# Optimization experiments

Measured on AMD Instinct MI355X. Metric: run time of the kernel, lower is better.

Reference implementation:

```python
import jax, jax.numpy as jnp
import numpy as np

N = 131072       # total nodes (B graphs x P nodes)
P = 4096         # nodes per graph
B = 32           # graphs in batch
E = 2097152      # edges (avg degree 16)
IN_DIM = 64
HID = 128
OUT = 16
EPS = 1e-5
SLOPE = 0.01


def _degrees(idx):
    # structural degree, clamped to min 1 (as DGL GraphConv does)
    d = jax.ops.segment_sum(jnp.ones((E,), jnp.float32), idx, num_segments=N)
    return jnp.maximum(d, 1.0)


def _graph_conv(x, W, src, dst, ew):
    # DGL GraphConv, norm='both', bias=False, with scalar edge weights:
    # h = D_out^{-1/2} x ; m_v = sum_{(u->v)} w_e h_u ; out = (D_in^{-1/2} m) W
    h = x * jax.lax.rsqrt(_degrees(src))[:, None]
    m = jax.ops.segment_sum(ew[:, None] * h[src], dst, num_segments=N)  # [N, F]
    return (m * jax.lax.rsqrt(_degrees(dst))[:, None]) @ W


def _graph_norm(x, gamma, beta, alpha):
    # GraphNorm (Cai et al. / PyG, batch=None): stats over all nodes per feature
    mu = jnp.mean(x, axis=0)
    c = x - alpha * mu
    var = jnp.mean(c * c, axis=0)
    return c * jax.lax.rsqrt(var + EPS) * gamma + beta


def _mean_nodes(h, gid):
    # per-graph mean readout; every graph has exactly P nodes
    return jax.ops.segment_sum(h, gid, num_segments=B) / P


def setup_inputs() -> dict:
    key = jax.random.key(0)
    ks = jax.random.split(key, 8)
    src = jax.random.randint(ks[0], (E,), 0, N, dtype=jnp.int32)
    # keep edges within each 4096-node graph block (batched DGL graph)
    dst = (src // P) * P + jax.random.randint(ks[1], (E,), 0, P, dtype=jnp.int32)
    features = jax.random.normal(ks[2], (N, IN_DIM), jnp.float32)
    edge_weights = jax.random.uniform(ks[3], (E,), jnp.float32)
    # kaiming/xavier-scale init approximations
    W1 = jax.random.normal(ks[4], (IN_DIM, HID), jnp.float32) * np.sqrt(2.0 / IN_DIM)
    W2 = jax.random.normal(ks[5], (HID, HID), jnp.float32) * np.sqrt(2.0 / HID)
    Wc = jax.random.normal(ks[6], (OUT, 2 * HID), jnp.float32) * np.sqrt(1.0 / (2 * HID))
    ones = jnp.ones((HID,), jnp.float32)
    zeros = jnp.zeros((HID,), jnp.float32)
    return {
        'features': features, 'edge_weights': edge_weights, 'src': src, 'dst': dst,
        'W1': W1, 'W2': W2, 'Wc': Wc,
        'gamma1': ones, 'beta1': zeros, 'alpha1': ones,
        'gamma2': ones, 'beta2': zeros, 'alpha2': ones,
    }


def reference(features, edge_weights, src, dst, W1, W2, Wc,
              gamma1, beta1, alpha1, gamma2, beta2, alpha2):
    gid = jnp.arange(N, dtype=jnp.int32) // P  # node -> graph id
    h1 = _graph_conv(features, W1, src, dst, edge_weights)
    h1 = jax.nn.leaky_relu(_graph_norm(h1, gamma1, beta1, alpha1), SLOPE)
    r1 = _mean_nodes(h1, gid)                  # [B, HID]
    h2 = _graph_conv(h1, W2, src, dst, edge_weights)
    h2 = jax.nn.leaky_relu(_graph_norm(h2, gamma2, beta2, alpha2), SLOPE)
    r2 = _mean_nodes(h2, gid)                  # [B, HID]
    readouts = jnp.concatenate([r1, r2], axis=1)  # [B, 2*HID]
    return readouts @ Wc.T                     # [B, OUT]
```

## Files before the change

### kernel.cpp

```cpp
#include <hip/hip_runtime.h>
#include <hip/hip_fp16.h>

constexpr int NN   = 131072;
constexpr int PP   = 4096;
constexpr int BG   = 32;
constexpr int EE   = 2097152;
constexpr int IND  = 64;
constexpr int HH   = 128;
constexpr int CAP  = 81920;
constexpr float EPSV   = 1e-5f;
constexpr float SLOPEV = 0.01f;

typedef short bf16x8 __attribute__((ext_vector_type(8)));
typedef float f32x4  __attribute__((ext_vector_type(4)));

__device__ __forceinline__ unsigned f2bf(float f) {
    unsigned u = __float_as_uint(f);
    return (u + 0x7FFFu + ((u >> 16) & 1u)) >> 16;
}
__device__ __forceinline__ unsigned pack2bf(float lo, float hi) {
    return f2bf(lo) | (f2bf(hi) << 16);
}
__device__ __forceinline__ float bflo(unsigned p) { return __uint_as_float(p << 16); }
__device__ __forceinline__ float bfhi(unsigned p) { return __uint_as_float(p & 0xFFFF0000u); }
__device__ __forceinline__ float w16(unsigned r) {
    return __half2float(__ushort_as_half((unsigned short)(r >> 16)));
}

template <int K>
__device__ __forceinline__ void packw_body(const float* __restrict__ W,
                                           unsigned short* __restrict__ pw, int t) {
    if (t >= K * 16) return;
    int lane = t & 63, nt = (t >> 6) & 7, kt = t >> 9;
    int kbase = kt * 32 + ((lane >> 4) & 3) * 8;
    int col   = nt * 16 + (lane & 15);
    for (int j = 0; j < 8; j++)
        pw[t * 8 + j] = (unsigned short)f2bf(W[(kbase + j) * HH + col]);
}

__global__ __launch_bounds__(256) void k_prep(const float* __restrict__ features,
                                              unsigned* __restrict__ fx,
                                              const float* __restrict__ W1,
                                              unsigned short* __restrict__ pw1,
                                              const float* __restrict__ W2,
                                              unsigned short* __restrict__ pw2,
                                              int* __restrict__ gcur,
                                              float* __restrict__ racc) {
    int b = blockIdx.x, t = threadIdx.x;
    if (b < 16384) {
        int i = b * 256 + t;
        float2 v = ((const float2*)features)[i];
        fx[i] = pack2bf(v.x, v.y);
        return;
    }
    if (b == 16384) {
        if (t < BG) gcur[t * 16] = t * CAP;
        for (int i = t; i < 2 * BG * HH; i += 256) racc[i] = 0.f;
        return;
    }
    if (b < 16389) { packw_body<64>(W1, pw1, (b - 16385) * 256 + t); return; }
    packw_body<128>(W2, pw2, (b - 16389) * 256 + t);
}

__global__ __launch_bounds__(256) void k_part(const int* __restrict__ src,
                                              const int* __restrict__ dst,
                                              const float* __restrict__ ew,
                                              int* __restrict__ gcur,
                                              uint2* __restrict__ recs) {
    __shared__ int cnt[32];
    __shared__ int start[32];
    __shared__ int gbase[32];
    __shared__ uint2 stage[4096];
    int t = threadIdx.x;
    int ebase = blockIdx.x * 4096;
    if (t < 32) cnt[t] = 0;
    __syncthreads();
    int es[16]; int ed[16]; float ev[16];
#pragma unroll
    for (int k = 0; k < 16; k++) {
        int e = ebase + k * 256 + t;
        es[k] = src[e]; ed[k] = dst[e]; ev[k] = ew[e];
        atomicAdd(&cnt[es[k] >> 12], 1);
    }
    __syncthreads();
    if (t == 0) {
        int run = 0;
        for (int g = 0; g < 32; g++) { start[g] = run; run += cnt[g]; }
    }
    __syncthreads();
    if (t < 32) {
        gbase[t] = atomicAdd(&gcur[t * 16], cnt[t]);
        cnt[t] = start[t];
    }
    __syncthreads();
#pragma unroll
    for (int k = 0; k < 16; k++) {
        int g = es[k] >> 12;
        int pos = atomicAdd(&cnt[g], 1);
        stage[pos] = make_uint2((unsigned)(es[k] & 4095) | ((unsigned)(ed[k] & 4095) << 12) |
                                ((unsigned)g << 24), __float_as_uint(ev[k]));
    }
    __syncthreads();
    for (int i = t; i < 4096; i += 256) {
        uint2 r = stage[i];
        int g = r.x >> 24;
        recs[gbase[g] + (i - start[g])] = r;
    }
}

__global__ __launch_bounds__(1024) void k_hist(const uint2* __restrict__ recs,
                                               const int* __restrict__ gcur,
                                               int* __restrict__ shist,
                                               int* __restrict__ dhist) {
    __shared__ int hs[4096];
    __shared__ int hd[4096];
    int t = threadIdx.x;
    int g = blockIdx.x >> 3, c = blockIdx.x & 7;
    int n = gcur[g * 16] - g * CAP;
    int lo = (n * c) >> 3, hi = (n * (c + 1)) >> 3;
    ((int4*)hs)[t] = make_int4(0, 0, 0, 0);
    ((int4*)hd)[t] = make_int4(0, 0, 0, 0);
    __syncthreads();
    const uint2* base = recs + (size_t)g * CAP;
    for (int i = lo + t; i < hi; i += 1024) {
        unsigned x = base[i].x;
        atomicAdd(&hs[x & 4095], 1);
        atomicAdd(&hd[(x >> 12) & 4095], 1);
    }
    __syncthreads();
    ((int4*)(shist + (size_t)blockIdx.x * 4096))[t] = ((int4*)hs)[t];
    ((int4*)(dhist + (size_t)blockIdx.x * 4096))[t] = ((int4*)hd)[t];
}

__global__ __launch_bounds__(1024) void k_offs(int* __restrict__ shist,
                                               int* __restrict__ dhist,
                                               float* __restrict__ rs_s,
                                               float* __restrict__ rsd,
                                               int* __restrict__ degd,
                                               int* __restrict__ offs) {
    __shared__ int partial[1024];
    int t = threadIdx.x, g = blockIdx.x;
    int sdeg[4] = {0, 0, 0, 0}, ddeg[4] = {0, 0, 0, 0};
#pragma unroll
    for (int c = 0; c < 8; c++) {
        int4 sv = ((const int4*)(shist + (size_t)(g * 8 + c) * 4096))[t];
        int4 dv = ((const int4*)(dhist + (size_t)(g * 8 + c) * 4096))[t];
        sdeg[0] += sv.x; sdeg[1] += sv.y; sdeg[2] += sv.z; sdeg[3] += sv.w;
        ddeg[0] += dv.x; ddeg[1] += dv.y; ddeg[2] += dv.z; ddeg[3] += dv.w;
    }
    int pdeg[4];
#pragma unroll
    for (int j = 0; j < 4; j++) {
        int idx = t * 4 + j;
        int vs = sdeg[j]; if (vs < 1) vs = 1;
        rs_s[g * PP + idx] = rsqrtf((float)vs);
        int vd = ddeg[j]; if (vd < 1) vd = 1;
        rsd[g * PP + idx]  = rsqrtf((float)vd);
        pdeg[j] = (ddeg[j] + 3) & ~3;
        degd[g * PP + idx] = pdeg[j];
    }
    partial[t] = pdeg[0] + pdeg[1] + pdeg[2] + pdeg[3];
    __syncthreads();
    for (int off = 1; off < 1024; off <<= 1) {
        int v = partial[t];
        int add = (t >= off) ? partial[t - off] : 0;
        __syncthreads();
        partial[t] = v + add;
        __syncthreads();
    }
    int run = (t == 0) ? 0 : partial[t - 1];
#pragma unroll
    for (int j = 0; j < 4; j++) {
        int idx = t * 4 + j;
        offs[g * PP + idx] = g * CAP + run;
        int nb = run;
        for (int c = 0; c < 8; c++) {
            size_t hidx = (size_t)(g * 8 + c) * 4096 + idx;
            int v = dhist[hidx];
            dhist[hidx] = nb;
            nb += v;
        }
        run += pdeg[j];
    }
}

__global__ __launch_bounds__(1024) void k_place(const uint2* __restrict__ recs,
                                                const int* __restrict__ gcur,
                                                const int* __restrict__ dhist,
                                                const float* __restrict__ rs_s,
                                                unsigned* __restrict__ csr2) {
    __shared__ int cur[4096];
    __shared__ float rss[4096];
    int t = threadIdx.x;
    int g = blockIdx.x >> 3, c = blockIdx.x & 7;
    int n = gcur[g * 16] - g * CAP;
    int lo = (n * c) >> 3, hi = (n * (c + 1)) >> 3;
    ((int4*)cur)[t] = ((const int4*)(dhist + (size_t)blockIdx.x * 4096))[t];
    ((float4*)rss)[t] = ((const float4*)(rs_s + (size_t)g * PP))[t];
    __syncthreads();
    const uint2* base = recs + (size_t)g * CAP;
    unsigned* cbase = csr2 + (size_t)g * CAP;
    for (int i = lo + t; i < hi; i += 1024) {
        uint2 r = base[i];
        int sl = r.x & 4095, dl = (r.x >> 12) & 4095;
        int pos = atomicAdd(&cur[dl], 1);
        float wf = __uint_as_float(r.y) * rss[sl];
        cbase[pos] = (unsigned)sl | ((unsigned)__half_as_ushort(__float2half(wf)) << 16);
    }
}

__global__ __launch_bounds__(256) void k_agg1(const unsigned* __restrict__ fx,
                                              const unsigned* __restrict__ csr2,
                                              const int* __restrict__ offs,
                                              const int* __restrict__ degd,
                                              const float* __restrict__ rsd,
                                              unsigned* __restrict__ m1) {
    int bid = blockIdx.x;
    int xcd = bid & 7, idx = bid >> 3;
    int g = xcd * 4 + (idx >> 9);
    int node0 = g * PP + (idx & 511) * 8;
    int lane = threadIdx.x & 63, wv = threadIdx.x >> 6;
    int half = lane >> 5, sl = lane & 31;
    int v = node0 + wv * 2 + half;
    int o = offs[v], cnt = degd[v];
    const unsigned* hp = fx + (size_t)((unsigned)(g * PP) * 32) + sl;
    float ax0 = 0.f, ay0 = 0.f, ax1 = 0.f, ay1 = 0.f;
    for (int i = 0; i < cnt; i += 4) {
        uint4 rr = *(const uint4*)(csr2 + o + i);
        unsigned g0 = hp[(rr.x & 4095) * 32];
        unsigned g1 = hp[(rr.y & 4095) * 32];
        unsigned g2 = hp[(rr.z & 4095) * 32];
        unsigned g3 = hp[(rr.w & 4095) * 32];
        float w0 = w16(rr.x), w1 = w16(rr.y), w2 = w16(rr.z), w3 = w16(rr.w);
        ax0 += w0 * bflo(g0); ay0 += w0 * bfhi(g0);
        ax1 += w1 * bflo(g1); ay1 += w1 * bfhi(g1);
        ax0 += w2 * bflo(g2); ay0 += w2 * bfhi(g2);
        ax1 += w3 * bflo(g3); ay1 += w3 * bfhi(g3);
    }
    float rd = rsd[v];
    m1[(size_t)v * 32 + sl] = pack2bf((ax0 + ax1) * rd, (ay0 + ay1) * rd);
}

__global__ __launch_bounds__(256) void k_agg2(const unsigned* __restrict__ h1,
                                              const unsigned* __restrict__ csr2,
                                              const int* __restrict__ offs,
                                              const int* __restrict__ degd,
                                              const float* __restrict__ rsd,
                                              unsigned* __restrict__ m2) {
    int bid = blockIdx.x;
    int xcd = bid & 7, idx = bid >> 3;
    int g = xcd * 4 + (idx >> 9);
    int node0 = g * PP + (idx & 511) * 4;
    int lane = threadIdx.x & 63, wv = threadIdx.x >> 6;
    int va = node0 + wv, vb = va + 2048;
    int oa = offs[va], ca = degd[va];
    int ob = offs[vb], cb = degd[vb];
    const unsigned* hp = h1 + (size_t)((unsigned)(g * PP) * 64) + lane;
    float A0 = 0.f, A1 = 0.f, B0 = 0.f, B1 = 0.f;
    int c0 = ca < cb ? ca : cb;
    int cm = ca < cb ? cb : ca;
    int i = 0;
    for (; i < c0; i += 4) {
        uint4 ra = *(const uint4*)(csr2 + oa + i);
        uint4 rb = *(const uint4*)(csr2 + ob + i);
        unsigned ga0 = hp[(ra.x & 4095) * 64];
        unsigned ga1 = hp[(ra.y & 4095) * 64];
        unsigned ga2 = hp[(ra.z & 4095) * 64];
        unsigned ga3 = hp[(ra.w & 4095) * 64];
        unsigned gb0 = hp[(rb.x & 4095) * 64];
        unsigned gb1 = hp[(rb.y & 4095) * 64];
        unsigned gb2 = hp[(rb.z & 4095) * 64];
        unsigned gb3 = hp[(rb.w & 4095) * 64];
        float wa0 = w16(ra.x), wa1 = w16(ra.y), wa2 = w16(ra.z), wa3 = w16(ra.w);
        float wb0 = w16(rb.x), wb1 = w16(rb.y), wb2 = w16(rb.z), wb3 = w16(rb.w);
        A0 += wa0 * bflo(ga0); A1 += wa0 * bfhi(ga0);
        A0 += wa1 * bflo(ga1); A1 += wa1 * bfhi(ga1);
        A0 += wa2 * bflo(ga2); A1 += wa2 * bfhi(ga2);
        A0 += wa3 * bflo(ga3); A1 += wa3 * bfhi(ga3);
        B0 += wb0 * bflo(gb0); B1 += wb0 * bfhi(gb0);
        B0 += wb1 * bflo(gb1); B1 += wb1 * bfhi(gb1);
        B0 += wb2 * bflo(gb2); B1 += wb2 * bfhi(gb2);
        B0 += wb3 * bflo(gb3); B1 += wb3 * bfhi(gb3);
    }
    if (i < cm) {
        int ot = (ca > cb) ? oa : ob;
        float E0 = 0.f, E1 = 0.f, F0 = 0.f, F1 = 0.f;
        for (; i < cm; i += 4) {
            uint4 rr = *(const uint4*)(csr2 + ot + i);
            unsigned g0 = hp[(rr.x & 4095) * 64];
            unsigned g1 = hp[(rr.y & 4095) * 64];
            unsigned g2 = hp[(rr.z & 4095) * 64];
            unsigned g3 = hp[(rr.w & 4095) * 64];
            float w0 = w16(rr.x), w1 = w16(rr.y), w2 = w16(rr.z), w3 = w16(rr.w);
            E0 += w0 * bflo(g0); E1 += w0 * bfhi(g0);
            F0 += w1 * bflo(g1); F1 += w1 * bfhi(g1);
            E0 += w2 * bflo(g2); E1 += w2 * bfhi(g2);
            F0 += w3 * bflo(g3); F1 += w3 * bfhi(g3);
        }
        if (ca > cb) { A0 += E0 + F0; A1 += E1 + F1; }
        else         { B0 += E0 + F0; B1 += E1 + F1; }
    }
    float rda = rsd[va], rdb = rsd[vb];
    m2[(size_t)va * 64 + lane] = pack2bf(A0 * rda, A1 * rda);
    m2[(size_t)vb * 64 + lane] = pack2bf(B0 * rdb, B1 * rdb);
}

template <int K>
__global__ __launch_bounds__(256) void k_gemm(const short* __restrict__ A,
                                              const short* __restrict__ PW,
                                              unsigned short* __restrict__ C,
                                              float* __restrict__ part) {
    __shared__ float s1[HH], s2[HH];
    int t = threadIdx.x;
    if (t < HH) { s1[t] = 0.f; s2[t] = 0.f; }
    __syncthreads();
    int wv = t >> 6, lane = t & 63;
    int tile = blockIdx.x * 4 + wv;
    int m = lane & 15, quad = lane >> 4;
    int row = tile * 16 + m;
    bf16x8 a[K / 32];
#pragma unroll
    for (int kt = 0; kt < K / 32; kt++)
        a[kt] = *(const bf16x8*)(A + (size_t)row * K + kt * 32 + quad * 8);
#pragma unroll
    for (int nt = 0; nt < 8; nt++) {
        f32x4 acc = {0.f, 0.f, 0.f, 0.f};
#pragma unroll
        for (int kt = 0; kt < K / 32; kt++) {
            bf16x8 b = *(const bf16x8*)(PW + ((size_t)(kt * 8 + nt) * 64 + lane) * 8);
            acc = __builtin_amdgcn_mfma_f32_16x16x32_bf16(a[kt], b, acc, 0, 0, 0);
        }
        int col = nt * 16 + m;
        int r0 = tile * 16 + quad * 4;
        float ps = 0.f, pq = 0.f;
#pragma unroll
        for (int r = 0; r < 4; r++) {
            C[(size_t)(r0 + r) * HH + col] = (unsigned short)f2bf(acc[r]);
            ps += acc[r]; pq += acc[r] * acc[r];
        }
        atomicAdd(&s1[col], ps);
        atomicAdd(&s2[col], pq);
    }
    __syncthreads();
    if (t < HH) {
        part[blockIdx.x * 256 + t]      = s1[t];
        part[blockIdx.x * 256 + HH + t] = s2[t];
    }
}

__global__ __launch_bounds__(256) void k_red(const float* __restrict__ part,
                                             float* __restrict__ pb) {
    int t = threadIdx.x, b = blockIdx.x;
    float s = 0.f;
    for (int r = 0; r < 32; r++) s += part[(size_t)(b * 32 + r) * 256 + t];
    pb[b * 256 + t] = s;
}

__global__ void k_coef(const float* __restrict__ pb, const float* __restrict__ gamma,
                       const float* __restrict__ beta, const float* __restrict__ alpha,
                       float* __restrict__ ab) {
    int t = threadIdx.x;
    float s = 0.f;
    for (int b = 0; b < 64; b++) s += pb[b * 256 + t];
    __shared__ float sh[256];
    sh[t] = s;
    __syncthreads();
    if (t < 128) {
        float mu = sh[t] * (1.f / NN);
        float e2 = sh[128 + t] * (1.f / NN);
        float al = alpha[t];
        float var = e2 - (2.f * al - al * al) * mu * mu;
        float a = rsqrtf(var + EPSV) * gamma[t];
        ab[t] = a;
        ab[HH + t] = beta[t] - al * mu * a;
    }
}

template <bool WRITE>
__global__ __launch_bounds__(256) void k_normro(unsigned* __restrict__ h,
                                                const float* __restrict__ ab,
                                                float* __restrict__ racc) {
    int fp = threadIdx.x & 63;
    int q  = threadIdx.x >> 6;
    int node0 = blockIdx.x * 64;
    int g = node0 / PP;
    float a0 = ab[2 * fp], a1 = ab[2 * fp + 1];
    float b0 = ab[HH + 2 * fp], b1 = ab[HH + 2 * fp + 1];
    float s0 = 0.f, s1 = 0.f;
    for (int i = q; i < 64; i += 4) {
        size_t idx = (size_t)(node0 + i) * 64 + fp;
        unsigned v = h[idx];
        float x0 = fmaf(a0, bflo(v), b0); x0 = x0 > 0.f ? x0 : SLOPEV * x0;
        float x1 = fmaf(a1, bfhi(v), b1); x1 = x1 > 0.f ? x1 : SLOPEV * x1;
        if (WRITE) h[idx] = pack2bf(x0, x1);
        s0 += x0; s1 += x1;
    }
    __shared__ float sh[512];
    sh[threadIdx.x] = s0;
    sh[256 + threadIdx.x] = s1;
    __syncthreads();
    if (q == 0) {
        float t0 = s0 + sh[64 + fp] + sh[128 + fp] + sh[192 + fp];
        float t1 = s1 + sh[256 + 64 + fp] + sh[256 + 128 + fp] + sh[256 + 192 + fp];
        atomicAdd(&racc[g * HH + 2 * fp],     t0);
        atomicAdd(&racc[g * HH + 2 * fp + 1], t1);
    }
}

__global__ void k_final(const float* __restrict__ racc1, const float* __restrict__ racc2,
                        const float* __restrict__ Wc, float* __restrict__ out) {
    int t = threadIdx.x;
    int b = t >> 4, o = t & 15;
    float acc = 0.f;
    for (int f = 0; f < HH; f++) acc += racc1[b * HH + f] * Wc[o * (2 * HH) + f];
    for (int f = 0; f < HH; f++) acc += racc2[b * HH + f] * Wc[o * (2 * HH) + HH + f];
    out[t] = acc * (1.f / PP);
}

extern "C" void kernel_launch(void* const* d_in, const int* in_sizes, int n_in,
                              void* d_out, int out_size, void* d_ws, size_t ws_size,
                              hipStream_t stream) {
    const float* features = (const float*)d_in[0];
    const float* ew       = (const float*)d_in[1];
    const int*   src      = (const int*)d_in[2];
    const int*   dst      = (const int*)d_in[3];
    const float* W1       = (const float*)d_in[4];
    const float* W2       = (const float*)d_in[5];
    const float* Wc       = (const float*)d_in[6];
    const float* gamma1   = (const float*)d_in[7];
    const float* beta1    = (const float*)d_in[8];
    const float* alpha1   = (const float*)d_in[9];
    const float* gamma2   = (const float*)d_in[10];
    const float* beta2    = (const float*)d_in[11];
    const float* alpha2   = (const float*)d_in[12];
    float* out = (float*)d_out;

    char* w = (char*)d_ws;
    int*    gcur   = (int*)(w + 0);
    float*  racc1  = (float*)(w + (16u << 10));
    float*  racc2  = (float*)(w + (32u << 10));
    float*  ab1    = (float*)(w + (48u << 10));
    float*  ab2    = (float*)(w + (52u << 10));
    unsigned short* pw1 = (unsigned short*)(w + (64u << 10));
    unsigned short* pw2 = (unsigned short*)(w + (80u << 10));
    float*  pb     = (float*)(w + (128u << 10));
    float*  rs_s   = (float*)(w + (1024u << 10));
    float*  rsd    = (float*)(w + (1536u << 10));
    int*    degd   = (int*)(w + (2048u << 10));
    int*    offs   = (int*)(w + (2560u << 10));
    float*  part   = (float*)(w + (3u << 20));
    int*    shist  = (int*)(w + (5u << 20));
    int*    dhist  = (int*)(w + (9u << 20));
    unsigned* csr2 = (unsigned*)(w + (13u << 20));
    unsigned* mbuf = (unsigned*)(w + (23u << 20));
    unsigned* hbuf = (unsigned*)(w + (55u << 20));
    uint2*    recs = (uint2*)(w + (87u << 20));
    unsigned* fx   = (unsigned*)(w + (107u << 20));

    k_prep<<<16397, 256, 0, stream>>>(features, fx, W1, pw1, W2, pw2, gcur, racc1);
    hipMemsetAsync(csr2, 0, (size_t)BG * CAP * sizeof(unsigned), stream);

    k_part<<<EE / 4096, 256, 0, stream>>>(src, dst, ew, gcur, recs);
    k_hist<<<BG * 8, 1024, 0, stream>>>(recs, gcur, shist, dhist);
    k_offs<<<BG, 1024, 0, stream>>>(shist, dhist, rs_s, rsd, degd, offs);
    k_place<<<BG * 8, 1024, 0, stream>>>(recs, gcur, dhist, rs_s, csr2);

    k_agg1<<<NN / 8, 256, 0, stream>>>(fx, csr2, offs, degd, rsd, mbuf);
    k_gemm<64><<<NN / 64, 256, 0, stream>>>((const short*)mbuf, (const short*)pw1,
                                            (unsigned short*)hbuf, part);
    k_red<<<64, 256, 0, stream>>>(part, pb);
    k_coef<<<1, 256, 0, stream>>>(pb, gamma1, beta1, alpha1, ab1);
    k_normro<true><<<NN / 64, 256, 0, stream>>>(hbuf, ab1, racc1);

    k_agg2<<<NN / 8, 256, 0, stream>>>(hbuf, csr2, offs, degd, rsd, mbuf);
    k_gemm<128><<<NN / 64, 256, 0, stream>>>((const short*)mbuf, (const short*)pw2,
                                             (unsigned short*)hbuf, part);
    k_red<<<64, 256, 0, stream>>>(part, pb);
    k_coef<<<1, 256, 0, stream>>>(pb, gamma2, beta2, alpha2, ab2);
    k_normro<false><<<NN / 64, 256, 0, stream>>>(hbuf, ab2, racc2);

    k_final<<<1, 512, 0, stream>>>(racc1, racc2, Wc, out);
}
```

Baseline: 412.8 us.

## Fuse neighbor aggregation with MFMA GEMM via LDS staging, fold csr2 memset into prep

Aggregation and the dense weight GEMM now run in one kernel per layer. Each block aggregates 64 nodes into a padded LDS tile and then runs bf16 MFMA directly from LDS, so the intermediate aggregated buffer no longer goes through global memory. The second layer writes to mbuf so that hbuf, which it reads from, is not overwritten. The csr2 zeroing moves from hipMemsetAsync into extra blocks of the prep kernel. In exchange the grid is 8x smaller, and each wave walks 8 sequential node groups, which lowers the parallelism available to hide gather latency.

```diff
diff --git a/kernel.cpp b/kernel.cpp
--- a/kernel.cpp
+++ b/kernel.cpp
@@ -45,7 +45,8 @@
                                               const float* __restrict__ W2,
                                               unsigned short* __restrict__ pw2,
                                               int* __restrict__ gcur,
-                                              float* __restrict__ racc) {
+                                              float* __restrict__ racc,
+                                              unsigned* __restrict__ csr2) {
     int b = blockIdx.x, t = threadIdx.x;
     if (b < 16384) {
         int i = b * 256 + t;
@@ -59,7 +60,8 @@
         return;
     }
     if (b < 16389) { packw_body<64>(W1, pw1, (b - 16385) * 256 + t); return; }
-    packw_body<128>(W2, pw2, (b - 16389) * 256 + t);
+    if (b < 16397) { packw_body<128>(W2, pw2, (b - 16389) * 256 + t); return; }
+    ((uint4*)csr2)[(b - 16397) * 256 + t] = make_uint4(0, 0, 0, 0);
 }
 
 __global__ __launch_bounds__(256) void k_part(const int* __restrict__ src,
@@ -209,129 +211,62 @@
     }
 }
 
-__global__ __launch_bounds__(256) void k_agg1(const unsigned* __restrict__ fx,
-                                              const unsigned* __restrict__ csr2,
-                                              const int* __restrict__ offs,
-                                              const int* __restrict__ degd,
-                                              const float* __restrict__ rsd,
-                                              unsigned* __restrict__ m1) {
+__global__ __launch_bounds__(256) void k_aggemm1(const unsigned* __restrict__ fx,
+                                                 const unsigned* __restrict__ csr2,
+                                                 const int* __restrict__ offs,
+                                                 const int* __restrict__ degd,
+                                                 const float* __restrict__ rsd,
+                                                 const short* __restrict__ PW,
+                                                 unsigned short* __restrict__ C,
+                                                 float* __restrict__ part) {
+    constexpr int WP = 36;
+    __shared__ unsigned lds[64 * WP];
+    __shared__ float s1[HH], s2[HH];
+    int t = threadIdx.x;
+    if (t < HH) { s1[t] = 0.f; s2[t] = 0.f; }
     int bid = blockIdx.x;
     int xcd = bid & 7, idx = bid >> 3;
-    int g = xcd * 4 + (idx >> 9);
-    int node0 = g * PP + (idx & 511) * 8;
-    int lane = threadIdx.x & 63, wv = threadIdx.x >> 6;
+    int g = xcd * 4 + (idx >> 6);
+    int node0 = g * PP + (idx & 63) * 64;
+    int lane = t & 63, wv = t >> 6;
     int half = lane >> 5, sl = lane & 31;
-    int v = node0 + wv * 2 + half;
-    int o = offs[v], cnt = degd[v];
     const unsigned* hp = fx + (size_t)((unsigned)(g * PP) * 32) + sl;
-    float ax0 = 0.f, ay0 = 0.f, ax1 = 0.f, ay1 = 0.f;
-    for (int i = 0; i < cnt; i += 4) {
-        uint4 rr = *(const uint4*)(csr2 + o + i);
-        unsigned g0 = hp[(rr.x & 4095) * 32];
-        unsigned g1 = hp[(rr.y & 4095) * 32];
-        unsigned g2 = hp[(rr.z & 4095) * 32];
-        unsigned g3 = hp[(rr.w & 4095) * 32];
-        float w0 = w16(rr.x), w1 = w16(rr.y), w2 = w16(rr.z), w3 = w16(rr.w);
-        ax0 += w0 * bflo(g0); ay0 += w0 * bfhi(g0);
-        ax1 += w1 * bflo(g1); ay1 += w1 * bfhi(g1);
-        ax0 += w2 * bflo(g2); ay0 += w2 * bfhi(g2);
-        ax1 += w3 * bflo(g3); ay1 += w3 * bfhi(g3);
-    }
-    float rd = rsd[v];
-    m1[(size_t)v * 32 + sl] = pack2bf((ax0 + ax1) * rd, (ay0 + ay1) * rd);
-}
-
-__global__ __launch_bounds__(256) void k_agg2(const unsigned* __restrict__ h1,
-                                              const unsigned* __restrict__ csr2,
-                                              const int* __restrict__ offs,
-                                              const int* __restrict__ degd,
-                                              const float* __restrict__ rsd,
-                                              unsigned* __restrict__ m2) {
-    int bid = blockIdx.x;
-    int xcd = bid & 7, idx = bid >> 3;
-    int g = xcd * 4 + (idx >> 9);
-    int node0 = g * PP + (idx & 511) * 4;
-    int lane = threadIdx.x & 63, wv = threadIdx.x >> 6;
-    int va = node0 + wv, vb = va + 2048;
-    int oa = offs[va], ca = degd[va];
-    int ob = offs[vb], cb = degd[vb];
-    const unsigned* hp = h1 + (size_t)((unsigned)(g * PP) * 64) + lane;
-    float A0 = 0.f, A1 = 0.f, B0 = 0.f, B1 = 0.f;
-    int c0 = ca < cb ? ca : cb;
-    int cm = ca < cb ? cb : ca;
-    int i = 0;
-    for (; i < c0; i += 4) {
-        uint4 ra = *(const uint4*)(csr2 + oa + i);
-        uint4 rb = *(const uint4*)(csr2 + ob + i);
-        unsigned ga0 = hp[(ra.x & 4095) * 64];
-        unsigned ga1 = hp[(ra.y & 4095) * 64];
-        unsigned ga2 = hp[(ra.z & 4095) * 64];
-        unsigned ga3 = hp[(ra.w & 4095) * 64];
-        unsigned gb0 = hp[(rb.x & 4095) * 64];
-        unsigned gb1 = hp[(rb.y & 4095) * 64];
-        unsigned gb2 = hp[(rb.z & 4095) * 64];
-        unsigned gb3 = hp[(rb.w & 4095) * 64];
-        float wa0 = w16(ra.x), wa1 = w16(ra.y), wa2 = w16(ra.z), wa3 = w16(ra.w);
-        float wb0 = w16(rb.x), wb1 = w16(rb.y), wb2 = w16(rb.z), wb3 = w16(rb.w);
-        A0 += wa0 * bflo(ga0); A1 += wa0 * bfhi(ga0);
-        A0 += wa1 * bflo(ga1); A1 += wa1 * bfhi(ga1);
-        A0 += wa2 * bflo(ga2); A1 += wa2 * bfhi(ga2);
-        A0 += wa3 * bflo(ga3); A1 += wa3 * bfhi(ga3);
-        B0 += wb0 * bflo(gb0); B1 += wb0 * bfhi(gb0);
-        B0 += wb1 * bflo(gb1); B1 += wb1 * bfhi(gb1);
-        B0 += wb2 * bflo(gb2); B1 += wb2 * bfhi(gb2);
-        B0 += wb3 * bflo(gb3); B1 += wb3 * bfhi(gb3);
-    }
-    if (i < cm) {
-        int ot = (ca > cb) ? oa : ob;
-        float E0 = 0.f, E1 = 0.f, F0 = 0.f, F1 = 0.f;
-        for (; i < cm; i += 4) {
-            uint4 rr = *(const uint4*)(csr2 + ot + i);
-            unsigned g0 = hp[(rr.x & 4095) * 64];
-            unsigned g1 = hp[(rr.y & 4095) * 64];
-            unsigned g2 = hp[(rr.z & 4095) * 64];
-            unsigned g3 = hp[(rr.w & 4095) * 64];
+    for (int p = 0; p < 8; p++) {
+        int lr = wv * 16 + p * 2 + half;
+        int v = node0 + lr;
+        int o = offs[v], cnt = degd[v];
+        float ax0 = 0.f, ay0 = 0.f, ax1 = 0.f, ay1 = 0.f;
+        for (int i = 0; i < cnt; i += 4) {
+            uint4 rr = *(const uint4*)(csr2 + o + i);
+            unsigned g0 = hp[(rr.x & 4095) * 32];
+            unsigned g1 = hp[(rr.y & 4095) * 32];
+            unsigned g2 = hp[(rr.z & 4095) * 32];
+            unsigned g3 = hp[(rr.w & 4095) * 32];
             float w0 = w16(rr.x), w1 = w16(rr.y), w2 = w16(rr.z), w3 = w16(rr.w);
-            E0 += w0 * bflo(g0); E1 += w0 * bfhi(g0);
-            F0 += w1 * bflo(g1); F1 += w1 * bfhi(g1);
-            E0 += w2 * bflo(g2); E1 += w2 * bfhi(g2);
-            F0 += w3 * bflo(g3); F1 += w3 * bfhi(g3);
-        }
-        if (ca > cb) { A0 += E0 + F0; A1 += E1 + F1; }
-        else         { B0 += E0 + F0; B1 += E1 + F1; }
-    }
-    float rda = rsd[va], rdb = rsd[vb];
-    m2[(size_t)va * 64 + lane] = pack2bf(A0 * rda, A1 * rda);
-    m2[(size_t)vb * 64 + lane] = pack2bf(B0 * rdb, B1 * rdb);
-}
-
-template <int K>
-__global__ __launch_bounds__(256) void k_gemm(const short* __restrict__ A,
-                                              const short* __restrict__ PW,
-                                              unsigned short* __restrict__ C,
-                                              float* __restrict__ part) {
-    __shared__ float s1[HH], s2[HH];
-    int t = threadIdx.x;
-    if (t < HH) { s1[t] = 0.f; s2[t] = 0.f; }
-    __syncthreads();
-    int wv = t >> 6, lane = t & 63;
-    int tile = blockIdx.x * 4 + wv;
+            ax0 += w0 * bflo(g0); ay0 += w0 * bfhi(g0);
+            ax1 += w1 * bflo(g1); ay1 += w1 * bfhi(g1);
+            ax0 += w2 * bflo(g2); ay0 += w2 * bfhi(g2);
+            ax1 += w3 * bflo(g3); ay1 += w3 * bfhi(g3);
+        }
+        float rd = rsd[v];
+        lds[lr * WP + sl] = pack2bf((ax0 + ax1) * rd, (ay0 + ay1) * rd);
+    }
+    __syncthreads();
     int m = lane & 15, quad = lane >> 4;
-    int row = tile * 16 + m;
-    bf16x8 a[K / 32];
-#pragma unroll
-    for (int kt = 0; kt < K / 32; kt++)
-        a[kt] = *(const bf16x8*)(A + (size_t)row * K + kt * 32 + quad * 8);
+    bf16x8 a[2];
+#pragma unroll
+    for (int kt = 0; kt < 2; kt++)
+        a[kt] = *(const bf16x8*)&lds[(wv * 16 + m) * WP + kt * 16 + quad * 4];
 #pragma unroll
     for (int nt = 0; nt < 8; nt++) {
         f32x4 acc = {0.f, 0.f, 0.f, 0.f};
 #pragma unroll
-        for (int kt = 0; kt < K / 32; kt++) {
+        for (int kt = 0; kt < 2; kt++) {
             bf16x8 b = *(const bf16x8*)(PW + ((size_t)(kt * 8 + nt) * 64 + lane) * 8);
             acc = __builtin_amdgcn_mfma_f32_16x16x32_bf16(a[kt], b, acc, 0, 0, 0);
         }
         int col = nt * 16 + m;
-        int r0 = tile * 16 + quad * 4;
+        int r0 = node0 + wv * 16 + quad * 4;
         float ps = 0.f, pq = 0.f;
 #pragma unroll
         for (int r = 0; r < 4; r++) {
@@ -343,8 +278,111 @@
     }
     __syncthreads();
     if (t < HH) {
-        part[blockIdx.x * 256 + t]      = s1[t];
-        part[blockIdx.x * 256 + HH + t] = s2[t];
+        part[bid * 256 + t]      = s1[t];
+        part[bid * 256 + HH + t] = s2[t];
+    }
+}
+
+__global__ __launch_bounds__(256) void k_aggemm2(const unsigned* __restrict__ h1,
+                                                 const unsigned* __restrict__ csr2,
+                                                 const int* __restrict__ offs,
+                                                 const int* __restrict__ degd,
+                                                 const float* __restrict__ rsd,
+                                                 const short* __restrict__ PW,
+                                                 unsigned short* __restrict__ C,
+                                                 float* __restrict__ part) {
+    constexpr int WP = 68;
+    __shared__ unsigned lds[64 * WP];
+    __shared__ float s1[HH], s2[HH];
+    int t = threadIdx.x;
+    if (t < HH) { s1[t] = 0.f; s2[t] = 0.f; }
+    int bid = blockIdx.x;
+    int xcd = bid & 7, idx = bid >> 3;
+    int g = xcd * 4 + (idx >> 6);
+    int node0 = g * PP + (idx & 63) * 64;
+    int lane = t & 63, wv = t >> 6;
+    const unsigned* hp = h1 + (size_t)((unsigned)(g * PP) * 64) + lane;
+    for (int p = 0; p < 8; p++) {
+        int va = node0 + wv * 16 + p, vb = va + 8;
+        int oa = offs[va], ca = degd[va];
+        int ob = offs[vb], cb = degd[vb];
+        float A0 = 0.f, A1 = 0.f, B0 = 0.f, B1 = 0.f;
+        int c0 = ca < cb ? ca : cb;
+        int cm = ca < cb ? cb : ca;
+        int i = 0;
+        for (; i < c0; i += 4) {
+            uint4 ra = *(const uint4*)(csr2 + oa + i);
+            uint4 rb = *(const uint4*)(csr2 + ob + i);
+            unsigned ga0 = hp[(ra.x & 4095) * 64];
+            unsigned ga1 = hp[(ra.y & 4095) * 64];
+            unsigned ga2 = hp[(ra.z & 4095) * 64];
+            unsigned ga3 = hp[(ra.w & 4095) * 64];
+            unsigned gb0 = hp[(rb.x & 4095) * 64];
+            unsigned gb1 = hp[(rb.y & 4095) * 64];
+            unsigned gb2 = hp[(rb.z & 4095) * 64];
+            unsigned gb3 = hp[(rb.w & 4095) * 64];
+            float wa0 = w16(ra.x), wa1 = w16(ra.y), wa2 = w16(ra.z), wa3 = w16(ra.w);
+            float wb0 = w16(rb.x), wb1 = w16(rb.y), wb2 = w16(rb.z), wb3 = w16(rb.w);
+            A0 += wa0 * bflo(ga0); A1 += wa0 * bfhi(ga0);
+            A0 += wa1 * bflo(ga1); A1 += wa1 * bfhi(ga1);
+            A0 += wa2 * bflo(ga2); A1 += wa2 * bfhi(ga2);
+            A0 += wa3 * bflo(ga3); A1 += wa3 * bfhi(ga3);
+            B0 += wb0 * bflo(gb0); B1 += wb0 * bfhi(gb0);
+            B0 += wb1 * bflo(gb1); B1 += wb1 * bfhi(gb1);
+            B0 += wb2 * bflo(gb2); B1 += wb2 * bfhi(gb2);
+            B0 += wb3 * bflo(gb3); B1 += wb3 * bfhi(gb3);
+        }
+        if (i < cm) {
+            int ot = (ca > cb) ? oa : ob;
+            float E0 = 0.f, E1 = 0.f, F0 = 0.f, F1 = 0.f;
+            for (; i < cm; i += 4) {
+                uint4 rr = *(const uint4*)(csr2 + ot + i);
+                unsigned g0 = hp[(rr.x & 4095) * 64];
+                unsigned g1 = hp[(rr.y & 4095) * 64];
+                unsigned g2 = hp[(rr.z & 4095) * 64];
+                unsigned g3 = hp[(rr.w & 4095) * 64];
+                float w0 = w16(rr.x), w1 = w16(rr.y), w2 = w16(rr.z), w3 = w16(rr.w);
+                E0 += w0 * bflo(g0); E1 += w0 * bfhi(g0);
+                F0 += w1 * bflo(g1); F1 += w1 * bfhi(g1);
+                E0 += w2 * bflo(g2); E1 += w2 * bfhi(g2);
+                F0 += w3 * bflo(g3); F1 += w3 * bfhi(g3);
+            }
+            if (ca > cb) { A0 += E0 + F0; A1 += E1 + F1; }
+            else         { B0 += E0 + F0; B1 += E1 + F1; }
+        }
+        float rda = rsd[va], rdb = rsd[vb];
+        lds[(wv * 16 + p) * WP + lane]     = pack2bf(A0 * rda, A1 * rda);
+        lds[(wv * 16 + p + 8) * WP + lane] = pack2bf(B0 * rdb, B1 * rdb);
+    }
+    __syncthreads();
+    int m = lane & 15, quad = lane >> 4;
+    bf16x8 a[4];
+#pragma unroll
+    for (int kt = 0; kt < 4; kt++)
+        a[kt] = *(const bf16x8*)&lds[(wv * 16 + m) * WP + kt * 16 + quad * 4];
+#pragma unroll
+    for (int nt = 0; nt < 8; nt++) {
+        f32x4 acc = {0.f, 0.f, 0.f, 0.f};
+#pragma unroll
+        for (int kt = 0; kt < 4; kt++) {
+            bf16x8 b = *(const bf16x8*)(PW + ((size_t)(kt * 8 + nt) * 64 + lane) * 8);
+            acc = __builtin_amdgcn_mfma_f32_16x16x32_bf16(a[kt], b, acc, 0, 0, 0);
+        }
+        int col = nt * 16 + m;
+        int r0 = node0 + wv * 16 + quad * 4;
+        float ps = 0.f, pq = 0.f;
+#pragma unroll
+        for (int r = 0; r < 4; r++) {
+            C[(size_t)(r0 + r) * HH + col] = (unsigned short)f2bf(acc[r]);
+            ps += acc[r]; pq += acc[r] * acc[r];
+        }
+        atomicAdd(&s1[col], ps);
+        atomicAdd(&s2[col], pq);
+    }
+    __syncthreads();
+    if (t < HH) {
+        part[bid * 256 + t]      = s1[t];
+        part[bid * 256 + HH + t] = s2[t];
     }
 }
 
@@ -457,27 +495,24 @@
     uint2*    recs = (uint2*)(w + (87u << 20));
     unsigned* fx   = (unsigned*)(w + (107u << 20));
 
-    k_prep<<<16397, 256, 0, stream>>>(features, fx, W1, pw1, W2, pw2, gcur, racc1);
-    hipMemsetAsync(csr2, 0, (size_t)BG * CAP * sizeof(unsigned), stream);
+    k_prep<<<18957, 256, 0, stream>>>(features, fx, W1, pw1, W2, pw2, gcur, racc1, csr2);
 
     k_part<<<EE / 4096, 256, 0, stream>>>(src, dst, ew, gcur, recs);
     k_hist<<<BG * 8, 1024, 0, stream>>>(recs, gcur, shist, dhist);
     k_offs<<<BG, 1024, 0, stream>>>(shist, dhist, rs_s, rsd, degd, offs);
     k_place<<<BG * 8, 1024, 0, stream>>>(recs, gcur, dhist, rs_s, csr2);
 
-    k_agg1<<<NN / 8, 256, 0, stream>>>(fx, csr2, offs, degd, rsd, mbuf);
-    k_gemm<64><<<NN / 64, 256, 0, stream>>>((const short*)mbuf, (const short*)pw1,
-                                            (unsigned short*)hbuf, part);
+    k_aggemm1<<<NN / 64, 256, 0, stream>>>(fx, csr2, offs, degd, rsd,
+                                           (const short*)pw1, (unsigned short*)hbuf, part);
     k_red<<<64, 256, 0, stream>>>(part, pb);
     k_coef<<<1, 256, 0, stream>>>(pb, gamma1, beta1, alpha1, ab1);
     k_normro<true><<<NN / 64, 256, 0, stream>>>(hbuf, ab1, racc1);
 
-    k_agg2<<<NN / 8, 256, 0, stream>>>(hbuf, csr2, offs, degd, rsd, mbuf);
-    k_gemm<128><<<NN / 64, 256, 0, stream>>>((const short*)mbuf, (const short*)pw2,
-                                             (unsigned short*)hbuf, part);
+    k_aggemm2<<<NN / 64, 256, 0, stream>>>(hbuf, csr2, offs, degd, rsd,
+                                           (const short*)pw2, (unsigned short*)mbuf, part);
     k_red<<<64, 256, 0, stream>>>(part, pb);
     k_coef<<<1, 256, 0, stream>>>(pb, gamma2, beta2, alpha2, ab2);
-    k_normro<false><<<NN / 64, 256, 0, stream>>>(hbuf, ab2, racc2);
+    k_normro<false><<<NN / 64, 256, 0, stream>>>(mbuf, ab2, racc2);
 
     k_final<<<1, 512, 0, stream>>>(racc1, racc2, Wc, out);
 }
```

New measurement: 391.0 us. 1.06x faster.
